# Optimization experiments

Measured on AMD Instinct MI355X. Metric: run time of the kernel, lower is better.

The kernel has to match this reference:

```python
import jax, jax.numpy as jnp
import numpy as np

RMS_EPS = 1e-6
B, S, H = 2, 4096, 4096
N_Q_OUT, N_KV_OUT = 4096, 1024  # 32 heads * 128, 8 kv heads * 128


def setup_inputs() -> dict:
    key = jax.random.key(0)
    k1, k2, k3, k4 = jax.random.split(key, 4)
    scale = 1.0 / np.sqrt(H)
    return {
        "hidden_states": jax.random.normal(k1, (B, S, H), dtype=jnp.float32),
        "gamma": jnp.ones((H,), dtype=jnp.float32),
        "w_q": jax.random.normal(k2, (H, N_Q_OUT), dtype=jnp.float32) * scale,
        "w_k": jax.random.normal(k3, (H, N_KV_OUT), dtype=jnp.float32) * scale,
        "w_v": jax.random.normal(k4, (H, N_KV_OUT), dtype=jnp.float32) * scale,
    }


def _rmsnorm(x, gamma, eps=RMS_EPS):
    # x: [B, S, H]; normalize over last axis
    var = jnp.mean(jnp.square(x), axis=-1, keepdims=True)
    return x * jax.lax.rsqrt(var + eps) * gamma


def reference(hidden_states, gamma, w_q, w_k, w_v):
    # Fused RMSNorm + QKV projection (GQA): normalize once, then three
    # column-parallel matmuls sharing the normalized activation.
    xn = _rmsnorm(hidden_states, gamma)  # [B, S, H]
    q = jnp.einsum("bsh,hd->bsd", xn, w_q)  # [B, S, n_heads*head_dim]
    k = jnp.einsum("bsh,hd->bsd", xn, w_k)  # [B, S, n_kv_heads*head_dim]
    v = jnp.einsum("bsh,hd->bsd", xn, w_v)  # [B, S, n_kv_heads*head_dim]
    return q, k, v
```

## Files before the change

kernel.cpp:

```cpp
#include <hip/hip_runtime.h>
#include <hip/hip_bf16.h>
#include <stdint.h>

#define HD      4096
#define MROWS   8192
#define NQ      4096
#define NKV     1024
#define NTOT    6144
#define RMS_EPS 1e-6f

typedef __attribute__((ext_vector_type(8))) short bf16x8;
typedef __attribute__((ext_vector_type(4))) float f32x4;

static __device__ __forceinline__ unsigned short f2bf(float f) {
  union { float f; unsigned u; } a; a.f = f;
  unsigned r = a.u + 0x7FFFu + ((a.u >> 16) & 1u);
  return (unsigned short)(r >> 16);
}

__global__ __launch_bounds__(256) void rmsnorm_cast_kernel(
    const float* __restrict__ x, const float* __restrict__ gamma,
    unsigned short* __restrict__ xn) {
  const int row = blockIdx.x;
  const float4* xr = (const float4*)(x + (size_t)row * HD);
  const float4* g4 = (const float4*)gamma;
  const int t = threadIdx.x;
  float4 v[4];
  float ss = 0.f;
#pragma unroll
  for (int i = 0; i < 4; ++i) {
    v[i] = xr[t + i * 256];
    ss += v[i].x * v[i].x + v[i].y * v[i].y + v[i].z * v[i].z + v[i].w * v[i].w;
  }
#pragma unroll
  for (int o = 32; o > 0; o >>= 1) ss += __shfl_xor(ss, o, 64);
  __shared__ float red[4];
  if ((t & 63) == 0) red[t >> 6] = ss;
  __syncthreads();
  const float tot = red[0] + red[1] + red[2] + red[3];
  const float rstd = rsqrtf(tot * (1.f / HD) + RMS_EPS);
  ushort4* xo = (ushort4*)(xn + (size_t)row * HD);
#pragma unroll
  for (int i = 0; i < 4; ++i) {
    const float4 g = g4[t + i * 256];
    ushort4 o;
    o.x = f2bf(v[i].x * rstd * g.x);
    o.y = f2bf(v[i].y * rstd * g.y);
    o.z = f2bf(v[i].z * rstd * g.z);
    o.w = f2bf(v[i].w * rstd * g.w);
    xo[t + i * 256] = o;
  }
}

__global__ __launch_bounds__(256) void transpose_cast_kernel(
    const float* __restrict__ w, unsigned short* __restrict__ wt, int Nw) {
  __shared__ float tile[32][33];
  const int kt = blockIdx.y;
  const int nb = blockIdx.x;
  const int t = threadIdx.x;
  const int r = t >> 3, c4 = t & 7;
  const float4 vin = *(const float4*)&w[(size_t)(kt * 32 + r) * Nw + nb * 32 + c4 * 4];
  tile[r][c4 * 4 + 0] = vin.x;
  tile[r][c4 * 4 + 1] = vin.y;
  tile[r][c4 * 4 + 2] = vin.z;
  tile[r][c4 * 4 + 3] = vin.w;
  __syncthreads();
  ushort4 o;
  o.x = f2bf(tile[c4 * 4 + 0][r]);
  o.y = f2bf(tile[c4 * 4 + 1][r]);
  o.z = f2bf(tile[c4 * 4 + 2][r]);
  o.w = f2bf(tile[c4 * 4 + 3][r]);
  *(ushort4*)&wt[(size_t)(nb * 32 + r) * HD + kt * 32 + c4 * 4] = o;
}


static __device__ __forceinline__ void gload_lds16(const unsigned short* g,
                                                   unsigned short* l) {
  __builtin_amdgcn_global_load_lds(
      (const __attribute__((address_space(1))) void*)g,
      (__attribute__((address_space(3))) void*)l, 16, 0, 0);
}

#define VM4 asm volatile("s_waitcnt vmcnt(4)" ::: "memory")
#define VM0 asm volatile("s_waitcnt vmcnt(0)" ::: "memory")
#define VMNONE ((void)0)

#define PHASE(BUF, HA, HB, VM, ...)                                            \
  do {                                                                         \
    const unsigned short* Ah = &lds[0][BUF][HA][0];                            \
    const unsigned short* Bh = &lds[1][BUF][HB][0];                            \
    bf16x8 af[4][2];                                                           \
    bf16x8 bfr[2][2];                                                          \
    _Pragma("unroll") for (int im = 0; im < 4; ++im) {                         \
      const int r = wr * 64 + im * 16 + fr;                                    \
      af[im][0] = *(const bf16x8*)((const char*)Ah + r * 128 + kb0);           \
      af[im][1] = *(const bf16x8*)((const char*)Ah + r * 128 + (kb0 ^ 64));    \
    }                                                                          \
    _Pragma("unroll") for (int jn = 0; jn < 2; ++jn) {                         \
      const int rb = wc * 32 + jn * 16 + fr;                                   \
      bfr[jn][0] = *(const bf16x8*)((const char*)Bh + rb * 128 + kb0);         \
      bfr[jn][1] = *(const bf16x8*)((const char*)Bh + rb * 128 + (kb0 ^ 64));  \
    }                                                                          \
    __VA_ARGS__;                                                               \
    __builtin_amdgcn_s_barrier();                                              \
    __builtin_amdgcn_s_setprio(1);                                             \
    _Pragma("unroll") for (int ks = 0; ks < 2; ++ks)                           \
      _Pragma("unroll") for (int im = 0; im < 4; ++im)                         \
        _Pragma("unroll") for (int jn = 0; jn < 2; ++jn)                       \
          acc[(HA) * 4 + im][(HB) * 2 + jn] =                                  \
              __builtin_amdgcn_mfma_f32_16x16x32_bf16(                         \
                  af[im][ks], bfr[jn][ks], acc[(HA) * 4 + im][(HB) * 2 + jn],  \
                  0, 0, 0);                                                    \
    __builtin_amdgcn_s_setprio(0);                                             \
    VM;                                                                        \
    __builtin_amdgcn_s_barrier();                                              \
  } while (0)

__global__ __launch_bounds__(512, 2) void gemm_qkv_kernel(
    const unsigned short* __restrict__ A,
    const unsigned short* __restrict__ Bt,
    float* __restrict__ out) {
  __shared__ unsigned short lds[2][2][2][8192] __attribute__((aligned(16)));

  const int bid = blockIdx.x;
  const int swz = (bid & 7) * 96 + (bid >> 3);
  const int mt = swz / 24, nt = swz % 24;
  const int m0 = mt * 256, n0 = nt * 256;

  const int tid = threadIdx.x;
  const int w = tid >> 6, lane = tid & 63;
  const int wr = w >> 2, wc = w & 3;
  const int fr = lane & 15, fq = lane >> 4;
  const int kb0 = ((lane >> 4) << 4) ^ ((fr & 7) << 4);

  const int wslot = w * 512;
  const int r3 = tid >> 3;
  const int scolb = ((tid & 7) << 4) ^ ((r3 & 7) << 4);
  const size_t so0 = (size_t)r3 * HD + (scolb >> 1);
  const size_t so1 = so0 + (size_t)64 * HD;

  const unsigned short* const Ab0 = A + (size_t)m0 * HD;
  const unsigned short* const Ab1 = Ab0 + (size_t)128 * HD;
  const unsigned short* const Bb0 = Bt + (size_t)n0 * HD;
  const unsigned short* const Bb1 = Bb0 + (size_t)128 * HD;

  auto STG = [&](const unsigned short* g, unsigned short* l) {
    gload_lds16(g + so0, l + wslot);
    gload_lds16(g + so1, l + 4096 + wslot);
  };

  f32x4 acc[8][4];
#pragma unroll
  for (int i = 0; i < 8; ++i)
#pragma unroll
    for (int j = 0; j < 4; ++j) acc[i][j] = (f32x4){0.f, 0.f, 0.f, 0.f};

  STG(Ab0, &lds[0][0][0][0]);
  STG(Bb0, &lds[1][0][0][0]);
  STG(Ab1, &lds[0][0][1][0]);
  STG(Bb1, &lds[1][0][1][0]);
  STG(Ab0 + 64, &lds[0][1][0][0]);
  STG(Bb0 + 64, &lds[1][1][0][0]);
  VM4;
  __builtin_amdgcn_s_barrier();

  for (int t = 0; t < 31; ++t) {
    const size_t k1 = (size_t)(2 * t + 1) * 64;
    const size_t o2 = (size_t)(2 * t + 2) * 64;
    const size_t o3 = (size_t)(2 * t + 3) * 64;
    PHASE(0, 0, 0, VMNONE, STG(Ab1 + k1, &lds[0][1][1][0]));
    PHASE(0, 0, 1, VMNONE, STG(Bb1 + k1, &lds[1][1][1][0]));
    PHASE(0, 1, 0, VMNONE, STG(Ab0 + o2, &lds[0][0][0][0]));
    PHASE(0, 1, 1, VM4,    STG(Bb0 + o2, &lds[1][0][0][0]));
    PHASE(1, 0, 0, VMNONE, STG(Ab1 + o2, &lds[0][0][1][0]));
    PHASE(1, 0, 1, VMNONE, STG(Bb1 + o2, &lds[1][0][1][0]));
    PHASE(1, 1, 0, VMNONE, STG(Ab0 + o3, &lds[0][1][0][0]));
    PHASE(1, 1, 1, VM4,    STG(Bb0 + o3, &lds[1][1][0][0]));
  }
  {
    const size_t k1 = (size_t)63 * 64;
    PHASE(0, 0, 0, VMNONE, STG(Ab1 + k1, &lds[0][1][1][0]));
    PHASE(0, 0, 1, VMNONE, STG(Bb1 + k1, &lds[1][1][1][0]));
    PHASE(0, 1, 0, VMNONE, VMNONE);
    PHASE(0, 1, 1, VM0,    VMNONE);
    PHASE(1, 0, 0, VMNONE, VMNONE);
    PHASE(1, 0, 1, VMNONE, VMNONE);
    PHASE(1, 1, 0, VMNONE, VMNONE);
    PHASE(1, 1, 1, VMNONE, VMNONE);
  }

  size_t obase; int ldc, nc;
  if (n0 < NQ)            { obase = 0;                                        ldc = NQ;  nc = n0; }
  else if (n0 < NQ + NKV) { obase = (size_t)MROWS * NQ;                       ldc = NKV; nc = n0 - NQ; }
  else                    { obase = (size_t)MROWS * NQ + (size_t)MROWS * NKV; ldc = NKV; nc = n0 - NQ - NKV; }

#pragma unroll
  for (int I = 0; I < 8; ++I) {
    const int rown = m0 + (I >> 2) * 128 + wr * 64 + (I & 3) * 16 + fq * 4;
#pragma unroll
    for (int J = 0; J < 4; ++J) {
      const int col = nc + (J >> 1) * 128 + wc * 32 + (J & 1) * 16 + fr;
#pragma unroll
      for (int jj = 0; jj < 4; ++jj)
        out[obase + (size_t)(rown + jj) * ldc + col] = acc[I][J][jj];
    }
  }
}

extern "C" void kernel_launch(void* const* d_in, const int* in_sizes, int n_in,
                              void* d_out, int out_size, void* d_ws, size_t ws_size,
                              hipStream_t stream) {
  const float* x     = (const float*)d_in[0];
  const float* gamma = (const float*)d_in[1];
  const float* wq    = (const float*)d_in[2];
  const float* wk    = (const float*)d_in[3];
  const float* wv    = (const float*)d_in[4];
  float* out = (float*)d_out;

  unsigned short* xn = (unsigned short*)d_ws;
  unsigned short* wt = xn + (size_t)MROWS * HD;

  rmsnorm_cast_kernel<<<MROWS, 256, 0, stream>>>(x, gamma, xn);
  transpose_cast_kernel<<<dim3(NQ / 32, HD / 32), 256, 0, stream>>>(wq, wt, NQ);
  transpose_cast_kernel<<<dim3(NKV / 32, HD / 32), 256, 0, stream>>>(
      wk, wt + (size_t)NQ * HD, NKV);
  transpose_cast_kernel<<<dim3(NKV / 32, HD / 32), 256, 0, stream>>>(
      wv, wt + (size_t)(NQ + NKV) * HD, NKV);
  gemm_qkv_kernel<<<(MROWS / 256) * (NTOT / 256), 512, 0, stream>>>(xn, wt, out);
}
```

Baseline: 453.2 us.

## Reuse A fragments across B halves and remap tiles to XCD-local blocks

Restructures the GEMM inner loop so that the A LDS fragments are loaded once per A half and reused for both B halves, instead of being reloaded in each phase. This cuts LDS read traffic. It also replaces the block-to-tile swizzle with a mapping that gives each XCD a contiguous 8x12 patch of output tiles, to improve L2 reuse of A and B rows. The trade-off is longer live ranges for the A fragments, which may raise register pressure.

```diff
diff --git a/kernel.cpp b/kernel.cpp
--- a/kernel.cpp
+++ b/kernel.cpp
@@ -85,23 +85,28 @@
 #define VM0 asm volatile("s_waitcnt vmcnt(0)" ::: "memory")
 #define VMNONE ((void)0)
 
-#define PHASE(BUF, HA, HB, VM, ...)                                            \
+#define READS_A(BUF, HA)                                                       \
   do {                                                                         \
     const unsigned short* Ah = &lds[0][BUF][HA][0];                            \
-    const unsigned short* Bh = &lds[1][BUF][HB][0];                            \
-    bf16x8 af[4][2];                                                           \
-    bf16x8 bfr[2][2];                                                          \
     _Pragma("unroll") for (int im = 0; im < 4; ++im) {                         \
       const int r = wr * 64 + im * 16 + fr;                                    \
       af[im][0] = *(const bf16x8*)((const char*)Ah + r * 128 + kb0);           \
       af[im][1] = *(const bf16x8*)((const char*)Ah + r * 128 + (kb0 ^ 64));    \
     }                                                                          \
+  } while (0)
+
+#define READS_B(BUF, HB)                                                       \
+  do {                                                                         \
+    const unsigned short* Bh = &lds[1][BUF][HB][0];                            \
     _Pragma("unroll") for (int jn = 0; jn < 2; ++jn) {                         \
       const int rb = wc * 32 + jn * 16 + fr;                                   \
       bfr[jn][0] = *(const bf16x8*)((const char*)Bh + rb * 128 + kb0);         \
       bfr[jn][1] = *(const bf16x8*)((const char*)Bh + rb * 128 + (kb0 ^ 64));  \
     }                                                                          \
-    __VA_ARGS__;                                                               \
+  } while (0)
+
+#define MMA(HA, HB, VM)                                                        \
+  do {                                                                         \
     __builtin_amdgcn_s_barrier();                                              \
     __builtin_amdgcn_s_setprio(1);                                             \
     _Pragma("unroll") for (int ks = 0; ks < 2; ++ks)                           \
@@ -116,6 +121,17 @@
     __builtin_amdgcn_s_barrier();                                              \
   } while (0)
 
+#define PAIR(BUF, HA, STG1, VM1, STG2, VM2)                                    \
+  do {                                                                         \
+    READS_A(BUF, HA);                                                          \
+    READS_B(BUF, 0);                                                           \
+    STG1;                                                                      \
+    MMA(HA, 0, VM1);                                                           \
+    READS_B(BUF, 1);                                                           \
+    STG2;                                                                      \
+    MMA(HA, 1, VM2);                                                           \
+  } while (0)
+
 __global__ __launch_bounds__(512, 2) void gemm_qkv_kernel(
     const unsigned short* __restrict__ A,
     const unsigned short* __restrict__ Bt,
@@ -123,8 +139,12 @@
   __shared__ unsigned short lds[2][2][2][8192] __attribute__((aligned(16)));
 
   const int bid = blockIdx.x;
-  const int swz = (bid & 7) * 96 + (bid >> 3);
-  const int mt = swz / 24, nt = swz % 24;
+  const int xcd = bid & 7;
+  const int idx = bid >> 3;
+  const int sr  = idx >> 5;
+  const int i32 = idx & 31;
+  const int mt  = (xcd >> 1) * 8 + (i32 >> 2);
+  const int nt  = (xcd & 1) * 12 + sr * 4 + (i32 & 3);
   const int m0 = mt * 256, n0 = nt * 256;
 
   const int tid = threadIdx.x;
@@ -154,6 +174,9 @@
   for (int i = 0; i < 8; ++i)
 #pragma unroll
     for (int j = 0; j < 4; ++j) acc[i][j] = (f32x4){0.f, 0.f, 0.f, 0.f};
+
+  bf16x8 af[4][2];
+  bf16x8 bfr[2][2];
 
   STG(Ab0, &lds[0][0][0][0]);
   STG(Bb0, &lds[1][0][0][0]);
@@ -168,25 +191,22 @@
     const size_t k1 = (size_t)(2 * t + 1) * 64;
     const size_t o2 = (size_t)(2 * t + 2) * 64;
     const size_t o3 = (size_t)(2 * t + 3) * 64;
-    PHASE(0, 0, 0, VMNONE, STG(Ab1 + k1, &lds[0][1][1][0]));
-    PHASE(0, 0, 1, VMNONE, STG(Bb1 + k1, &lds[1][1][1][0]));
-    PHASE(0, 1, 0, VMNONE, STG(Ab0 + o2, &lds[0][0][0][0]));
-    PHASE(0, 1, 1, VM4,    STG(Bb0 + o2, &lds[1][0][0][0]));
-    PHASE(1, 0, 0, VMNONE, STG(Ab1 + o2, &lds[0][0][1][0]));
-    PHASE(1, 0, 1, VMNONE, STG(Bb1 + o2, &lds[1][0][1][0]));
-    PHASE(1, 1, 0, VMNONE, STG(Ab0 + o3, &lds[0][1][0][0]));
-    PHASE(1, 1, 1, VM4,    STG(Bb0 + o3, &lds[1][1][0][0]));
+    PAIR(0, 0, STG(Ab1 + k1, &lds[0][1][1][0]), VMNONE,
+               STG(Bb1 + k1, &lds[1][1][1][0]), VMNONE);
+    PAIR(0, 1, STG(Ab0 + o2, &lds[0][0][0][0]), VMNONE,
+               STG(Bb0 + o2, &lds[1][0][0][0]), VM4);
+    PAIR(1, 0, STG(Ab1 + o2, &lds[0][0][1][0]), VMNONE,
+               STG(Bb1 + o2, &lds[1][0][1][0]), VMNONE);
+    PAIR(1, 1, STG(Ab0 + o3, &lds[0][1][0][0]), VMNONE,
+               STG(Bb0 + o3, &lds[1][1][0][0]), VM4);
   }
   {
     const size_t k1 = (size_t)63 * 64;
-    PHASE(0, 0, 0, VMNONE, STG(Ab1 + k1, &lds[0][1][1][0]));
-    PHASE(0, 0, 1, VMNONE, STG(Bb1 + k1, &lds[1][1][1][0]));
-    PHASE(0, 1, 0, VMNONE, VMNONE);
-    PHASE(0, 1, 1, VM0,    VMNONE);
-    PHASE(1, 0, 0, VMNONE, VMNONE);
-    PHASE(1, 0, 1, VMNONE, VMNONE);
-    PHASE(1, 1, 0, VMNONE, VMNONE);
-    PHASE(1, 1, 1, VMNONE, VMNONE);
+    PAIR(0, 0, STG(Ab1 + k1, &lds[0][1][1][0]), VMNONE,
+               STG(Bb1 + k1, &lds[1][1][1][0]), VMNONE);
+    PAIR(0, 1, VMNONE, VMNONE, VMNONE, VM0);
+    PAIR(1, 0, VMNONE, VMNONE, VMNONE, VMNONE);
+    PAIR(1, 1, VMNONE, VMNONE, VMNONE, VMNONE);
   }
 
   size_t obase; int ldc, nc;
```

New measurement: 409.9 us. 9.6% less time.
